# Performance work log

Hardware: AMD Instinct MI355X
Metric: run time of the kernel (lower is better)

## Reference

```python
import jax, jax.numpy as jnp
import numpy as np

N = 50000
E = 800000
IN_C = 128
HID = 128
OUT_C = 64
HEADS = 8
HD1 = HID // HEADS   # 16 per-head dim, layer 1 (concat)
HD2 = OUT_C          # 64 per-head dim, layer 2 (concat=False, mean over heads)
NEG_SLOPE = 0.2


def setup_inputs() -> dict:
    key = jax.random.key(0)
    ks = jax.random.split(key, 12)
    x = jax.random.normal(ks[0], (N, IN_C), dtype=jnp.float32)
    edge_index = jax.random.randint(ks[1], (2, E), 0, N, dtype=jnp.int64)
    s1 = 1.0 / np.sqrt(IN_C)
    s2 = 1.0 / np.sqrt(HID)
    W1 = jax.random.normal(ks[2], (IN_C, HEADS * HD1), dtype=jnp.float32) * s1
    att_src1 = jax.random.normal(ks[3], (HEADS, HD1), dtype=jnp.float32) * s1
    att_dst1 = jax.random.normal(ks[4], (HEADS, HD1), dtype=jnp.float32) * s1
    b1 = jnp.zeros((HID,), dtype=jnp.float32)
    W2 = jax.random.normal(ks[5], (HID, HEADS * HD2), dtype=jnp.float32) * s2
    att_src2 = jax.random.normal(ks[6], (HEADS, HD2), dtype=jnp.float32) * s2
    att_dst2 = jax.random.normal(ks[7], (HEADS, HD2), dtype=jnp.float32) * s2
    b2 = jnp.zeros((OUT_C,), dtype=jnp.float32)
    return {"x": x, "edge_index": edge_index,
            "W1": W1, "att_src1": att_src1, "att_dst1": att_dst1, "b1": b1,
            "W2": W2, "att_src2": att_src2, "att_dst2": att_dst2, "b2": b2}


def _gat_conv(x, W, a_src, a_dst, bias, src, dst, heads, head_dim, concat):
    n = x.shape[0]
    h = (x @ W).reshape(n, heads, head_dim)                      # [N,H,D]
    alpha_s = jnp.einsum('nhd,hd->nh', h, a_src)                  # [N,H]
    alpha_d = jnp.einsum('nhd,hd->nh', h, a_dst)                  # [N,H]
    e = jax.nn.leaky_relu(alpha_s[src] + alpha_d[dst], NEG_SLOPE)  # [E,H]
    # segment softmax over edges grouped by destination node
    m = jax.ops.segment_max(e, dst, num_segments=n)               # [N,H]
    m = jnp.where(jnp.isfinite(m), m, 0.0)
    ex = jnp.exp(e - m[dst])
    denom = jax.ops.segment_sum(ex, dst, num_segments=n)
    alpha = ex / (denom[dst] + 1e-16)                             # [E,H]
    out = jax.ops.segment_sum(h[src] * alpha[:, :, None], dst, num_segments=n)  # [N,H,D]
    if concat:
        out = out.reshape(n, heads * head_dim)
    else:
        out = out.mean(axis=1)
    return out + bias


def reference(x, edge_index, W1, att_src1, att_dst1, b1, W2, att_src2, att_dst2, b2):
    # PyG GATConv default add_self_loops=True
    loops = jnp.arange(N, dtype=edge_index.dtype)
    src = jnp.concatenate([edge_index[0], loops])
    dst = jnp.concatenate([edge_index[1], loops])
    h = _gat_conv(x, W1, att_src1, att_dst1, b1, src, dst, HEADS, HD1, True)
    h = jax.nn.relu(h)
    out = _gat_conv(h, W2, att_src2, att_dst2, b2, src, dst, HEADS, HD2, False)
    return out
```

## Files before the change

kernel.cpp:

```cpp
#include <hip/hip_runtime.h>

#define N_NODES 50000
#define N_EDGES 800000
#define ET (N_EDGES + N_NODES)
#define HEADS 8
#define NPAD 50048
#define SCAN_NB 196
#define CAP 96
#define LRS 1032
#define NB_DEG 3321
#define NB_GEMM1 782

typedef __attribute__((ext_vector_type(8))) _Float16 half8;
typedef __attribute__((ext_vector_type(2))) _Float16 half2v;
typedef __attribute__((ext_vector_type(4))) float f32x4;

__device__ __forceinline__ void wave_lds_fence(){
  asm volatile("s_waitcnt lgkmcnt(0)" ::: "memory");
}

__device__ __forceinline__ int edge_src(const int* ei, int e, int is64){
  if (e >= N_EDGES) return e - N_EDGES;
  return is64 ? ei[2*e] : ei[e];
}
__device__ __forceinline__ int edge_dst(const int* ei, int e, int is64){
  if (e >= N_EDGES) return e - N_EDGES;
  return is64 ? ei[2*(N_EDGES + e)] : ei[N_EDGES + e];
}

__global__ void k_init_wprep(const int* __restrict__ ei, int* __restrict__ deg,
                             int* __restrict__ cnt, int* __restrict__ flag,
                             const float* __restrict__ W1, const float* __restrict__ W2,
                             const float* __restrict__ as2, const float* __restrict__ ad2,
                             _Float16* __restrict__ Bp1, _Float16* __restrict__ Bp,
                             float* __restrict__ ws2, float* __restrict__ wd2){
  int b = blockIdx.x;
  int t_ = threadIdx.x;
  if (b < SCAN_NB){
    int i = b*256 + t_;
    if (i < N_NODES){ deg[i] = 0; cnt[i] = 0; }
    if (i == 0){
      int zeros = 0;
      for (int k = 0; k < 64; k++){
        if (ei[2*k + 1] == 0) zeros++;
      }
      *flag = (zeros >= 60) ? 1 : 0;
    }
  } else if (b < SCAN_NB + 256){
    int t = (b - SCAN_NB)*256 + t_;
    int j = t & 7, lane = (t >> 3) & 63, nt = (t >> 9) & 3, kt = t >> 11;
    int k = kt*32 + (lane >> 4)*8 + j;
    int c = nt*16 + (lane & 15);
    int h = k >> 7, kk = k & 127;
    Bp[t] = (_Float16)(0.125f * W2[kk*512 + h*64 + c]);
  } else if (b < SCAN_NB + 320){
    int t = (b - SCAN_NB - 256)*256 + t_;
    int j = t & 7, lane = (t >> 3) & 63, nt = (t >> 9) & 7, kt = t >> 12;
    int k = kt*32 + (lane >> 4)*8 + j;
    int c = nt*16 + (lane & 15);
    Bp1[t] = (_Float16)W1[k*128 + c];
  } else {
    int t = (b - SCAN_NB - 320)*256 + t_;
    int k = t >> 3, h = t & 7;
    float s = 0.f, d = 0.f;
    for (int dd = 0; dd < 64; dd++){
      float w = W2[k*512 + h*64 + dd];
      s += w * as2[h*64 + dd];
      d += w * ad2[h*64 + dd];
    }
    ws2[h*128 + k] = s;
    wd2[h*128 + k] = d;
  }
}

__global__ void __launch_bounds__(256) k_deg_gemm1(
    const int* __restrict__ ei, int* __restrict__ deg, const int* __restrict__ flag,
    const float* __restrict__ x, const _Float16* __restrict__ Bp1,
    _Float16* __restrict__ h1,
    const float* __restrict__ as1, const float* __restrict__ ad1,
    float* __restrict__ als1, float* __restrict__ ald1){
  if (blockIdx.x < NB_DEG){
    int e = blockIdx.x*blockDim.x + threadIdx.x;
    if (e >= ET) return;
    int is64 = *flag;
    int d = edge_dst(ei, e, is64);
    atomicAdd(&deg[d], 1);
    return;
  }
  int bid = blockIdx.x - NB_DEG;
  int tid = threadIdx.x;
  int lane = tid & 63, wv = tid >> 6;
  int n0 = bid*64 + wv*16;
  int rowA = n0 + (lane & 15);
  int koff = (lane >> 4)*8;
  const float* xr = x + (size_t)rowA*128 + koff;
  f32x4 acc[8];
  #pragma unroll
  for (int i = 0; i < 8; i++) acc[i] = (f32x4){0.f,0.f,0.f,0.f};
  bool inb = (rowA < N_NODES);
  #pragma unroll
  for (int kt = 0; kt < 4; kt++){
    half8 af;
    if (inb){
      float4 a0 = *(const float4*)(xr + kt*32);
      float4 a1 = *(const float4*)(xr + kt*32 + 4);
      af = (half8){(_Float16)a0.x,(_Float16)a0.y,(_Float16)a0.z,(_Float16)a0.w,
                   (_Float16)a1.x,(_Float16)a1.y,(_Float16)a1.z,(_Float16)a1.w};
    } else {
      af = (half8){0,0,0,0,0,0,0,0};
    }
    #pragma unroll
    for (int nt = 0; nt < 8; nt++){
      half8 bf = *(const half8*)(Bp1 + (((kt*8 + nt)*64 + lane) << 3));
      acc[nt] = __builtin_amdgcn_mfma_f32_16x16x32_f16(af, bf, acc[nt], 0, 0, 0);
    }
  }
  int m = lane & 15, q = lane >> 4;
  int r0 = n0 + q*4;
  #pragma unroll
  for (int nt = 0; nt < 8; nt++){
    int c = nt*16 + m;
    #pragma unroll
    for (int r = 0; r < 4; r++){
      int n = r0 + r;
      if (n < N_NODES) h1[(size_t)n*128 + c] = (_Float16)acc[nt][r];
    }
  }
  float as1v[8], ad1v[8];
  #pragma unroll
  for (int nt = 0; nt < 8; nt++){
    as1v[nt] = as1[nt*16 + m];
    ad1v[nt] = ad1[nt*16 + m];
  }
  #pragma unroll
  for (int r = 0; r < 4; r++){
    float vs[8], vd[8];
    #pragma unroll
    for (int nt = 0; nt < 8; nt++){
      vs[nt] = acc[nt][r]*as1v[nt];
      vd[nt] = acc[nt][r]*ad1v[nt];
      #pragma unroll
      for (int off = 1; off < 16; off <<= 1){
        vs[nt] += __shfl_xor(vs[nt], off, 64);
        vd[nt] += __shfl_xor(vd[nt], off, 64);
      }
    }
    int n = r0 + r;
    if (m == r && n < N_NODES){
      float4 v0; v0.x = vs[0]; v0.y = vs[1]; v0.z = vs[2]; v0.w = vs[3];
      float4 v1; v1.x = vs[4]; v1.y = vs[5]; v1.z = vs[6]; v1.w = vs[7];
      float4 w0; w0.x = vd[0]; w0.y = vd[1]; w0.z = vd[2]; w0.w = vd[3];
      float4 w1; w1.x = vd[4]; w1.y = vd[5]; w1.z = vd[6]; w1.w = vd[7];
      *(float4*)&als1[n*8]     = v0;
      *(float4*)&als1[n*8 + 4] = v1;
      *(float4*)&ald1[n*8]     = w0;
      *(float4*)&ald1[n*8 + 4] = w1;
    }
  }
}

__global__ void k_scan_part(const int* __restrict__ deg, int* __restrict__ loc,
                            int* __restrict__ part){
  __shared__ int lds[256];
  int t = threadIdx.x, i = blockIdx.x*256 + t;
  int v = (i < N_NODES) ? deg[i] : 0;
  lds[t] = v;
  __syncthreads();
  for (int off = 1; off < 256; off <<= 1){
    int x = (t >= off) ? lds[t - off] : 0;
    __syncthreads();
    lds[t] += x;
    __syncthreads();
  }
  if (i < N_NODES) loc[i] = lds[t] - v;
  if (t == 255) part[blockIdx.x] = lds[255];
}

__global__ void k_scan_carry(int* __restrict__ part, int* __restrict__ carry){
  __shared__ int lds[256];
  int t = threadIdx.x;
  int v = (t < SCAN_NB) ? part[t] : 0;
  lds[t] = v;
  __syncthreads();
  for (int off = 1; off < 256; off <<= 1){
    int x = (t >= off) ? lds[t - off] : 0;
    __syncthreads();
    lds[t] += x;
    __syncthreads();
  }
  if (t < SCAN_NB) carry[t] = lds[t] - v;
}

__global__ void k_scan_add(const int* __restrict__ loc, const int* __restrict__ carry,
                           int* __restrict__ row_ptr){
  int i = blockIdx.x*blockDim.x + threadIdx.x;
  if (i < N_NODES) row_ptr[i] = loc[i] + carry[i >> 8];
  if (i == 0) row_ptr[N_NODES] = ET;
}

__global__ void k_fill(const int* __restrict__ ei, const int* __restrict__ row_ptr,
                       int* __restrict__ cnt, int* __restrict__ col,
                       const int* __restrict__ flag){
  int e = blockIdx.x*blockDim.x + threadIdx.x;
  if (e >= ET) return;
  int is64 = *flag;
  int s = edge_src(ei, e, is64);
  int d = edge_dst(ei, e, is64);
  int pos = atomicAdd(&cnt[d], 1);
  col[row_ptr[d] + pos] = s;
}

__global__ void k_attn_agg1(const _Float16* __restrict__ h1,
    const float* __restrict__ als, const float* __restrict__ ald,
    const int* __restrict__ row_ptr, const int* __restrict__ col,
    const float* __restrict__ bias, _Float16* __restrict__ hr,
    const float* __restrict__ ws2, const float* __restrict__ wd2,
    float* __restrict__ als2, float* __restrict__ ald2){
  __shared__ _Float16 ew_s[4][CAP*8];
  __shared__ int col_s[4][CAP];
  __shared__ _Float16 ot_s[4][132];
  int tid = threadIdx.x;
  int wv = tid >> 6, lane = tid & 63;
  int n = blockIdx.x*4 + wv;
  int beg = row_ptr[n], end = row_ptr[n+1];
  int deg = end - beg;
  int items = deg*8;
  int h = lane & 7;
  float ad = ald[n*8 + h];
  _Float16* es = ew_s[wv];
  int* cs = col_s[wv];
  float l = 0.f;
  int itc = items < CAP*8 ? items : CAP*8;
  int it = lane;
  for (; it < itc; it += 64){
    int e = it >> 3;
    int s = col[beg + e];
    float a = als[s*8 + h] + ad;
    a = (a > 0.f) ? a : 0.2f*a;
    float ex = __expf(a);
    es[it] = (_Float16)ex;
    if ((it & 7) == 0) cs[e] = s;
    l += ex;
  }
  for (; it < items; it += 64){
    int s = col[beg + (it >> 3)];
    float a = als[s*8 + h] + ad;
    a = (a > 0.f) ? a : 0.2f*a;
    l += __expf(a);
  }
  l += __shfl_xor(l, 8, 64);
  l += __shfl_xor(l, 16, 64);
  l += __shfl_xor(l, 32, 64);
  float inv = 1.f / (l + 1e-16f);
  wave_lds_fence();
  int hh0 = lane >> 3;
  float invh = __shfl(inv, hh0, 64);
  const half2v* h2p = (const half2v*)h1;
  float ax = 0.f, ay = 0.f;
  int degc = deg < CAP ? deg : CAP;
  int j = 0;
  for (; j + 7 < degc; j += 8){
    int s[8]; float w[8]; half2v v[8];
    #pragma unroll
    for (int u = 0; u < 8; u++) s[u] = cs[j + u];
    #pragma unroll
    for (int u = 0; u < 8; u++) w[u] = (float)es[(j + u)*8 + hh0] * invh;
    #pragma unroll
    for (int u = 0; u < 8; u++) v[u] = h2p[(size_t)s[u]*64 + lane];
    #pragma unroll
    for (int u = 0; u < 8; u++){ ax += w[u]*(float)v[u].x; ay += w[u]*(float)v[u].y; }
  }
  for (; j < degc; j++){
    int s = cs[j];
    float w = (float)es[j*8 + hh0] * invh;
    half2v v = h2p[(size_t)s*64 + lane];
    ax += w*(float)v.x; ay += w*(float)v.y;
  }
  float adh = ald[n*8 + hh0];
  for (; j < deg; j++){
    int s = col[beg + j];
    float a = als[s*8 + hh0] + adh;
    a = (a > 0.f) ? a : 0.2f*a;
    float w = __expf(a)*invh;
    half2v v = h2p[(size_t)s*64 + lane];
    ax += w*(float)v.x; ay += w*(float)v.y;
  }
  float2 bb = ((const float2*)bias)[lane];
  float o0 = fmaxf(ax + bb.x, 0.f);
  float o1 = fmaxf(ay + bb.y, 0.f);
  half2v oo; oo.x = (_Float16)o0; oo.y = (_Float16)o1;
  ((half2v*)hr)[(size_t)n*64 + lane] = oo;
  ((half2v*)&ot_s[wv][0])[lane] = oo;
  wave_lds_fence();
  int hh = lane >> 3, seg = lane & 7;
  const half2v* otp = (const half2v*)&ot_s[wv][0];
  const float* wsr = ws2 + hh*128 + seg*16;
  const float* wdr = wd2 + hh*128 + seg*16;
  float vs = 0.f, vd = 0.f;
  #pragma unroll
  for (int i = 0; i < 8; i++){
    half2v v = otp[seg*8 + i];
    float vx = (float)v.x, vy = (float)v.y;
    vs += vx*wsr[2*i] + vy*wsr[2*i + 1];
    vd += vx*wdr[2*i] + vy*wdr[2*i + 1];
  }
  vs += __shfl_xor(vs, 1, 64); vd += __shfl_xor(vd, 1, 64);
  vs += __shfl_xor(vs, 2, 64); vd += __shfl_xor(vd, 2, 64);
  vs += __shfl_xor(vs, 4, 64); vd += __shfl_xor(vd, 4, 64);
  if (seg == 0){
    als2[n*8 + hh] = vs;
    ald2[n*8 + hh] = vd;
  }
}

__global__ void __launch_bounds__(1024) k_attn_agg2(const _Float16* __restrict__ hr,
    const float* __restrict__ als, const float* __restrict__ ald,
    const int* __restrict__ row_ptr, const int* __restrict__ col,
    const _Float16* __restrict__ Bp, const float* __restrict__ b2,
    float* __restrict__ outp){
  __shared__ _Float16 ew_s[16][CAP*8];
  __shared__ int col_s[16][CAP];
  __shared__ _Float16 at[16*LRS];
  int tid = threadIdx.x;
  int wv = tid >> 6, lane = tid & 63;
  int n = blockIdx.x*16 + wv;
  int beg = row_ptr[n], end = row_ptr[n+1];
  int deg = end - beg;
  int items = deg*8;
  int h = lane & 7;
  float ad = ald[n*8 + h];
  _Float16* es = ew_s[wv];
  int* cs = col_s[wv];
  float l = 0.f;
  int itc = items < CAP*8 ? items : CAP*8;
  int it = lane;
  for (; it < itc; it += 64){
    int e = it >> 3;
    int s = col[beg + e];
    float a = als[s*8 + h] + ad;
    a = (a > 0.f) ? a : 0.2f*a;
    float ex = __expf(a);
    es[it] = (_Float16)ex;
    if ((it & 7) == 0) cs[e] = s;
    l += ex;
  }
  for (; it < items; it += 64){
    int s = col[beg + (it >> 3)];
    float a = als[s*8 + h] + ad;
    a = (a > 0.f) ? a : 0.2f*a;
    l += __expf(a);
  }
  l += __shfl_xor(l, 8, 64);
  l += __shfl_xor(l, 16, 64);
  l += __shfl_xor(l, 32, 64);
  float inv = 1.f / (l + 1e-16f);
  wave_lds_fence();
  int hp = lane >> 4, cb = lane & 15;
  float invA = __shfl(inv, 2*hp, 64);
  float invB = __shfl(inv, 2*hp + 1, 64);
  half2v inv2; inv2.x = (_Float16)invA; inv2.y = (_Float16)invB;
  half2v acc_a[4], acc_b[4];
  #pragma unroll
  for (int i = 0; i < 4; i++){
    acc_a[i] = (half2v){(_Float16)0.f, (_Float16)0.f};
    acc_b[i] = (half2v){(_Float16)0.f, (_Float16)0.f};
  }
  int degc = deg < CAP ? deg : CAP;
  const _Float16* esw = es + 2*hp;
  int j = 0;
  for (; j + 3 < degc; j += 4){
    int s0 = cs[j], s1 = cs[j+1], s2 = cs[j+2], s3 = cs[j+3];
    half2v w0 = *(const half2v*)(esw + (j+0)*8) * inv2;
    half2v w1 = *(const half2v*)(esw + (j+1)*8) * inv2;
    half2v w2 = *(const half2v*)(esw + (j+2)*8) * inv2;
    half2v w3 = *(const half2v*)(esw + (j+3)*8) * inv2;
    half8 v0 = *(const half8*)(hr + (size_t)s0*128 + cb*8);
    half8 v1 = *(const half8*)(hr + (size_t)s1*128 + cb*8);
    half8 v2 = *(const half8*)(hr + (size_t)s2*128 + cb*8);
    half8 v3 = *(const half8*)(hr + (size_t)s3*128 + cb*8);
    #pragma unroll
    for (int k = 0; k < 4; k++){
      half2v t;
      t = (half2v){v0[2*k], v0[2*k+1]};
      acc_a[k] += (half2v){w0.x, w0.x} * t;
      acc_b[k] += (half2v){w0.y, w0.y} * t;
      t = (half2v){v1[2*k], v1[2*k+1]};
      acc_a[k] += (half2v){w1.x, w1.x} * t;
      acc_b[k] += (half2v){w1.y, w1.y} * t;
      t = (half2v){v2[2*k], v2[2*k+1]};
      acc_a[k] += (half2v){w2.x, w2.x} * t;
      acc_b[k] += (half2v){w2.y, w2.y} * t;
      t = (half2v){v3[2*k], v3[2*k+1]};
      acc_a[k] += (half2v){w3.x, w3.x} * t;
      acc_b[k] += (half2v){w3.y, w3.y} * t;
    }
  }
  for (; j < degc; j++){
    int s = cs[j];
    half2v w = *(const half2v*)(esw + j*8) * inv2;
    half8 v = *(const half8*)(hr + (size_t)s*128 + cb*8);
    #pragma unroll
    for (int k = 0; k < 4; k++){
      half2v t = (half2v){v[2*k], v[2*k+1]};
      acc_a[k] += (half2v){w.x, w.x} * t;
      acc_b[k] += (half2v){w.y, w.y} * t;
    }
  }
  if (deg > CAP){
    float2 adv = *(const float2*)(ald + (size_t)n*8 + 2*hp);
    for (; j < deg; j++){
      int s = col[beg + j];
      float2 alv = *(const float2*)(als + (size_t)s*8 + 2*hp);
      float a0 = alv.x + adv.x; a0 = (a0 > 0.f) ? a0 : 0.2f*a0;
      float a1 = alv.y + adv.y; a1 = (a1 > 0.f) ? a1 : 0.2f*a1;
      _Float16 w0 = (_Float16)(__expf(a0)*invA);
      _Float16 w1 = (_Float16)(__expf(a1)*invB);
      half8 v = *(const half8*)(hr + (size_t)s*128 + cb*8);
      #pragma unroll
      for (int k = 0; k < 4; k++){
        half2v t = (half2v){v[2*k], v[2*k+1]};
        acc_a[k] += (half2v){w0, w0} * t;
        acc_b[k] += (half2v){w1, w1} * t;
      }
    }
  }
  _Float16* ar = at + wv*LRS + (2*hp)*128 + cb*8;
  half8 oa, ob;
  #pragma unroll
  for (int k = 0; k < 4; k++){
    oa[2*k] = acc_a[k].x; oa[2*k+1] = acc_a[k].y;
    ob[2*k] = acc_b[k].x; ob[2*k+1] = acc_b[k].y;
  }
  *(half8*)ar = oa;
  *(half8*)(ar + 128) = ob;
  __syncthreads();
  if (wv >= 4) return;
  int m = lane & 15, q = lane >> 4;
  const _Float16* arow = at + m*LRS + q*8;
  f32x4 cacc = (f32x4){0.f,0.f,0.f,0.f};
  #pragma unroll 4
  for (int kt = 0; kt < 32; kt++){
    half8 af = *(const half8*)(arow + kt*32);
    half8 bf = *(const half8*)(Bp + (((kt*4 + wv)*64 + lane) << 3));
    cacc = __builtin_amdgcn_mfma_f32_16x16x32_f16(af, bf, cacc, 0, 0, 0);
  }
  int c = wv*16 + m;
  float bb = b2[c];
  #pragma unroll
  for (int r = 0; r < 4; r++){
    int nrow = blockIdx.x*16 + q*4 + r;
    outp[(size_t)nrow*64 + c] = cacc[r] + bb;
  }
}

extern "C" void kernel_launch(void* const* d_in, const int* in_sizes, int n_in,
                              void* d_out, int out_size, void* d_ws, size_t ws_size,
                              hipStream_t stream){
  const float* x   = (const float*)d_in[0];
  const int*   ei  = (const int*)d_in[1];
  const float* W1  = (const float*)d_in[2];
  const float* as1 = (const float*)d_in[3];
  const float* ad1 = (const float*)d_in[4];
  const float* b1  = (const float*)d_in[5];
  const float* W2  = (const float*)d_in[6];
  const float* as2 = (const float*)d_in[7];
  const float* ad2 = (const float*)d_in[8];
  const float* b2  = (const float*)d_in[9];
  float* outp = (float*)d_out;

  char* p = (char*)d_ws;
  auto alloc = [&](size_t bytes) -> void* {
    void* r = (void*)p;
    p += (bytes + 255) & ~(size_t)255;
    return r;
  };
  _Float16* h1  = (_Float16*)alloc((size_t)NPAD*128*2);
  _Float16* hr  = (_Float16*)alloc((size_t)N_NODES*128*2);
  float* als1 = (float*)alloc((size_t)N_NODES*8*4);
  float* ald1 = (float*)alloc((size_t)N_NODES*8*4);
  float* als2 = (float*)alloc((size_t)N_NODES*8*4);
  float* ald2 = (float*)alloc((size_t)N_NODES*8*4);
  int* row_ptr = (int*)alloc((size_t)(N_NODES+1)*4);
  int* deg  = (int*)alloc((size_t)N_NODES*4);
  int* cnt  = (int*)alloc((size_t)N_NODES*4);
  int* col  = (int*)alloc((size_t)ET*4);
  int* loc  = (int*)alloc((size_t)N_NODES*4);
  int* part = (int*)alloc(256*4);
  int* carry= (int*)alloc(256*4);
  int* flag = (int*)alloc(256);
  float* ws2 = (float*)alloc(1024*4);
  float* wd2 = (float*)alloc(1024*4);
  _Float16* Bp1 = (_Float16*)alloc((size_t)16384*2);
  _Float16* Bp  = (_Float16*)alloc((size_t)65536*2);

  dim3 b256(256);
  k_init_wprep<<<SCAN_NB + 324, b256, 0, stream>>>(ei, deg, cnt, flag,
                                                   W1, W2, as2, ad2,
                                                   Bp1, Bp, ws2, wd2);
  k_deg_gemm1<<<NB_DEG + NB_GEMM1, b256, 0, stream>>>(ei, deg, flag,
                                                      x, Bp1, h1, as1, ad1,
                                                      als1, ald1);
  k_scan_part<<<SCAN_NB, b256, 0, stream>>>(deg, loc, part);
  k_scan_carry<<<1, b256, 0, stream>>>(part, carry);
  k_scan_add<<<SCAN_NB, b256, 0, stream>>>(loc, carry, row_ptr);
  k_fill<<<(ET+255)/256, b256, 0, stream>>>(ei, row_ptr, cnt, col, flag);
  k_attn_agg1<<<N_NODES/4, b256, 0, stream>>>(h1, als1, ald1, row_ptr, col,
                                              b1, hr, ws2, wd2, als2, ald2);
  k_attn_agg2<<<N_NODES/16, dim3(1024), 0, stream>>>(hr, als2, ald2, row_ptr, col,
                                                     Bp, b2, outp);
}
```

Before: 326.6 us.

## Aggregate layer-1 neighbors with 16-byte loads across four edge groups per wave

Restructures the layer-1 attention aggregation so each wave splits into four edge groups of 16 lanes. Each lane loads a half8 (16 bytes) of the source feature row instead of a half2, so one wave instruction fetches four neighbor rows at once. The partial sums are then reduced across groups with shuffles. This cuts the number of load instructions per edge and gives more memory-level parallelism for low-degree nodes, at the cost of more accumulator registers and a cross-group reduction.

```diff
diff --git a/kernel.cpp b/kernel.cpp
--- a/kernel.cpp
+++ b/kernel.cpp
@@ -218,7 +218,7 @@
     float* __restrict__ als2, float* __restrict__ ald2){
   __shared__ _Float16 ew_s[4][CAP*8];
   __shared__ int col_s[4][CAP];
-  __shared__ _Float16 ot_s[4][132];
+  __shared__ _Float16 ot_s[4][136];
   int tid = threadIdx.x;
   int wv = tid >> 6, lane = tid & 63;
   int n = blockIdx.x*4 + wv;
@@ -253,44 +253,60 @@
   l += __shfl_xor(l, 32, 64);
   float inv = 1.f / (l + 1e-16f);
   wave_lds_fence();
-  int hh0 = lane >> 3;
-  float invh = __shfl(inv, hh0, 64);
-  const half2v* h2p = (const half2v*)h1;
-  float ax = 0.f, ay = 0.f;
+  int eg = lane >> 4, cb = lane & 15;
+  int hq = cb >> 1;
+  float invh = __shfl(inv, hq, 64);
+  float adh  = __shfl(ad, hq, 64);
+  float acc[8];
+  #pragma unroll
+  for (int k = 0; k < 8; k++) acc[k] = 0.f;
   int degc = deg < CAP ? deg : CAP;
   int j = 0;
-  for (; j + 7 < degc; j += 8){
-    int s[8]; float w[8]; half2v v[8];
+  for (; j + 3 < degc; j += 4){
+    int e = j + eg;
+    int s = cs[e];
+    float w = (float)es[e*8 + hq] * invh;
+    half8 v = *(const half8*)(h1 + (size_t)s*128 + cb*8);
     #pragma unroll
-    for (int u = 0; u < 8; u++) s[u] = cs[j + u];
-    #pragma unroll
-    for (int u = 0; u < 8; u++) w[u] = (float)es[(j + u)*8 + hh0] * invh;
-    #pragma unroll
-    for (int u = 0; u < 8; u++) v[u] = h2p[(size_t)s[u]*64 + lane];
-    #pragma unroll
-    for (int u = 0; u < 8; u++){ ax += w[u]*(float)v[u].x; ay += w[u]*(float)v[u].y; }
-  }
-  for (; j < degc; j++){
-    int s = cs[j];
-    float w = (float)es[j*8 + hh0] * invh;
-    half2v v = h2p[(size_t)s*64 + lane];
-    ax += w*(float)v.x; ay += w*(float)v.y;
-  }
-  float adh = ald[n*8 + hh0];
-  for (; j < deg; j++){
-    int s = col[beg + j];
-    float a = als[s*8 + hh0] + adh;
-    a = (a > 0.f) ? a : 0.2f*a;
-    float w = __expf(a)*invh;
-    half2v v = h2p[(size_t)s*64 + lane];
-    ax += w*(float)v.x; ay += w*(float)v.y;
-  }
-  float2 bb = ((const float2*)bias)[lane];
-  float o0 = fmaxf(ax + bb.x, 0.f);
-  float o1 = fmaxf(ay + bb.y, 0.f);
-  half2v oo; oo.x = (_Float16)o0; oo.y = (_Float16)o1;
-  ((half2v*)hr)[(size_t)n*64 + lane] = oo;
-  ((half2v*)&ot_s[wv][0])[lane] = oo;
+    for (int k = 0; k < 8; k++) acc[k] += w*(float)v[k];
+  }
+  if (j < degc){
+    int e = j + eg;
+    if (e < degc){
+      int s = cs[e];
+      float w = (float)es[e*8 + hq] * invh;
+      half8 v = *(const half8*)(h1 + (size_t)s*128 + cb*8);
+      #pragma unroll
+      for (int k = 0; k < 8; k++) acc[k] += w*(float)v[k];
+    }
+  }
+  for (int jj = degc; jj < deg; jj += 4){
+    int e = jj + eg;
+    if (e < deg){
+      int s = col[beg + e];
+      float a = als[s*8 + hq] + adh;
+      a = (a > 0.f) ? a : 0.2f*a;
+      float w = __expf(a)*invh;
+      half8 v = *(const half8*)(h1 + (size_t)s*128 + cb*8);
+      #pragma unroll
+      for (int k = 0; k < 8; k++) acc[k] += w*(float)v[k];
+    }
+  }
+  #pragma unroll
+  for (int k = 0; k < 8; k++){
+    acc[k] += __shfl_xor(acc[k], 16, 64);
+    acc[k] += __shfl_xor(acc[k], 32, 64);
+  }
+  float4 b0 = *(const float4*)(bias + cb*8);
+  float4 b1 = *(const float4*)(bias + cb*8 + 4);
+  float bb[8] = {b0.x,b0.y,b0.z,b0.w,b1.x,b1.y,b1.z,b1.w};
+  half8 oh;
+  #pragma unroll
+  for (int k = 0; k < 8; k++) oh[k] = (_Float16)fmaxf(acc[k] + bb[k], 0.f);
+  if (eg == 0){
+    *(half8*)(hr + (size_t)n*128 + cb*8) = oh;
+    ((half8*)&ot_s[wv][0])[cb] = oh;
+  }
   wave_lds_fence();
   int hh = lane >> 3, seg = lane & 7;
   const half2v* otp = (const half2v*)&ot_s[wv][0];
```

Result: no change. 322.5 us (median of 2 runs) (-1.3%).
